# Kernel optimization log

Measured on AMD Instinct MI355X. Metric: run time of the kernel, lower is better.

## Reference

```python
import jax, jax.numpy as jnp
import numpy as np

ST_HIDDEN = 128
ST_HEADS = 4
ST_LAYERS = 3
RES_SCALE = 1.0
DK = ST_HIDDEN // ST_HEADS


def build_3d_adj(spatial_ei, spatial_ea, n_nodes, window):
    # replicate spatial edges per time slice with node offset t*n_nodes
    offs = (jnp.arange(window) * n_nodes)[None, :, None]  # [1,W,1]
    all_sp_idx = (spatial_ei[:, None, :] + offs).reshape(2, -1)  # [2, W*E]
    all_sp_attr = jnp.tile(spatial_ea, (window, 1))  # [W*E, De]
    # temporal edges t -> t+1 for every node
    src = jnp.arange((window - 1) * n_nodes)
    temp_idx = jnp.stack([src, src + n_nodes], axis=0)  # [2, (W-1)*N]
    temp_attr = jnp.broadcast_to(spatial_ea.mean(axis=0, keepdims=True),
                                 (temp_idx.shape[1], spatial_ea.shape[1]))
    ei = jnp.concatenate([all_sp_idx, temp_idx], axis=1)
    ea = jnp.concatenate([all_sp_attr, temp_attr], axis=0)
    return ei, ea


def seg_softmax(logits, dst, num_nodes):
    # logits [E,H], segment softmax over dst (pyg_softmax)
    m = jax.ops.segment_max(logits, dst, num_segments=num_nodes)  # [N,H]
    ex = jnp.exp(logits - m[dst])
    s = jax.ops.segment_sum(ex, dst, num_segments=num_nodes)
    return ex / (s[dst] + 1e-16)


def layernorm(x, g, b, eps=1e-5):
    mu = x.mean(-1, keepdims=True)
    var = ((x - mu) ** 2).mean(-1, keepdims=True)
    return (x - mu) * jax.lax.rsqrt(var + eps) * g + b


def block(x, ei, ea, qw, qb, kw, kb, vw, vb, fw, fb, ow, ob, ln_g, ln_b):
    B, Nt, _ = x.shape
    H, dk = ST_HEADS, DK
    Q = (x @ qw + qb).reshape(B, Nt, H, dk)
    K = (x @ kw + kb).reshape(B, Nt, H, dk)
    V = (x @ vw + vb).reshape(B, Nt, H, dk)
    src, dst = ei[0], ei[1]
    q_e = Q[:, dst]  # [B,E,H,dk]
    k_e = K[:, src]
    v_e = V[:, src]
    film = ea @ fw + fb  # [E, 2*hidden]
    gamma, beta = jnp.split(film, 2, axis=-1)
    gamma = gamma.reshape(1, -1, H, dk)
    beta = beta.reshape(1, -1, H, dk)
    k_e = k_e * (1.0 + gamma) + beta
    logits = (q_e * k_e).sum(-1) / np.sqrt(dk).astype(np.float32)  # [B,E,H]
    att = jax.vmap(lambda l: seg_softmax(l, dst, Nt))(logits)
    msg = att[..., None] * v_e  # [B,E,H,dk]
    out = jnp.zeros((B, Nt, H, dk), x.dtype).at[:, dst].add(msg)
    y = out.reshape(B, Nt, H * dk) @ ow + ob
    return layernorm(x + y, ln_g, ln_b)


def setup_inputs() -> dict:
    key = jax.random.key(0)
    ks = jax.random.split(key, 12)
    B, W, N, Fin, E, De = 2, 16, 1000, 16, 16000, 8
    H, L = ST_HIDDEN, ST_LAYERS
    g = lambda k, s: jax.random.normal(k, s, jnp.float32) * 0.05
    return {
        "xw": jax.random.normal(ks[0], (B, W, N, Fin), jnp.float32),
        "spatial_ei": jax.random.randint(ks[1], (2, E), 0, N),
        "spatial_ea": jax.random.normal(ks[2], (E, De), jnp.float32),
        "in_w": g(ks[3], (Fin, H)), "in_b": jnp.zeros((H,), jnp.float32),
        "qw": g(ks[4], (L, H, H)), "qb": jnp.zeros((L, H), jnp.float32),
        "kw": g(ks[5], (L, H, H)), "kb": jnp.zeros((L, H), jnp.float32),
        "vw": g(ks[6], (L, H, H)), "vb": jnp.zeros((L, H), jnp.float32),
        "fw": g(ks[7], (L, De, 2 * H)), "fb": jnp.zeros((L, 2 * H), jnp.float32),
        "ow": g(ks[8], (L, H, H)), "ob": jnp.zeros((L, H), jnp.float32),
        "ln_g": jnp.ones((L, H), jnp.float32), "ln_b": jnp.zeros((L, H), jnp.float32),
        "head_w": g(ks[9], (H, 1)), "head_b": jnp.zeros((1,), jnp.float32),
    }


def reference(xw, spatial_ei, spatial_ea, in_w, in_b, qw, qb, kw, kb, vw, vb,
              fw, fb, ow, ob, ln_g, ln_b, head_w, head_b):
    B, W, N, Fin = xw.shape
    ei, ea = build_3d_adj(spatial_ei, spatial_ea, N, W)
    x = xw.reshape(B, W * N, Fin) @ in_w + in_b
    for l in range(ST_LAYERS):
        bx = block(x, ei, ea, qw[l], qb[l], kw[l], kb[l], vw[l], vb[l],
                   fw[l], fb[l], ow[l], ob[l], ln_g[l], ln_b[l])
        x = x + RES_SCALE * (bx - x)
    last = x.reshape(B, W, N, -1)[:, -1]  # [B,N,H]
    return jax.nn.softplus(last @ head_w + head_b).squeeze(-1)  # [B,N]
```

## Files before the change

### kernel.cpp

```cpp
#include <hip/hip_runtime.h>
#include <math.h>

constexpr int B    = 2;
constexpr int W    = 16;
constexpr int N    = 1000;
constexpr int FIN  = 16;
constexpr int E    = 16000;
constexpr int DE   = 8;
constexpr int H    = 128;
constexpr int L    = 3;
constexpr int WL   = 4;
constexpr int W0G  = 12;
constexpr int RPB  = WL * N;
constexpr int ROWS = B * RPB;
constexpr int NMAT = 12;

__device__ __forceinline__ float blockSum128(float v) {
  #pragma unroll
  for (int off = 32; off >= 1; off >>= 1) v += __shfl_xor(v, off);
  __shared__ float s2[2];
  int w = threadIdx.x >> 6;
  __syncthreads();
  if ((threadIdx.x & 63) == 0) s2[w] = v;
  __syncthreads();
  return s2[0] + s2[1];
}

__device__ __forceinline__ float dpp_add_xor1(float x) {
  int y = __builtin_amdgcn_update_dpp(0, __float_as_int(x), 0xB1, 0xF, 0xF, true);
  return x + __int_as_float(y);
}
__device__ __forceinline__ float dpp_add_xor2(float x) {
  int y = __builtin_amdgcn_update_dpp(0, __float_as_int(x), 0x4E, 0xF, 0xF, true);
  return x + __int_as_float(y);
}
__device__ __forceinline__ float headSum32(float p) {
  p = dpp_add_xor1(p);
  p = dpp_add_xor2(p);
  p += __shfl_xor(p, 4);
  p += __shfl_xor(p, 8);
  p += __shfl_xor(p, 16);
  return p;
}
__device__ __forceinline__ float dot4(float4 a, float4 b) {
  return a.x * b.x + a.y * b.y + a.z * b.z + a.w * b.w;
}

__global__ void k_hist(const int* __restrict__ ei, int* __restrict__ cnt,
                       const float* __restrict__ ea, float* __restrict__ meanea) {
  int bid = blockIdx.x;
  int t = threadIdx.x;
  if (bid < 64) {
    int e = bid * 256 + t;
    if (e < E) atomicAdd(&cnt[ei[E + e]], 1);
  } else {
    __shared__ float sbuf[256];
    int d = t & 7, g = t >> 3;
    float s = 0.f;
    for (int e = (bid - 64) * 32 + g; e < E; e += 64 * 32) s += ea[(long)e * DE + d];
    sbuf[t] = s;
    __syncthreads();
    for (int st = 16; st >= 1; st >>= 1) {
      if (g < st) sbuf[g * 8 + d] += sbuf[(g + st) * 8 + d];
      __syncthreads();
    }
    if (g == 0) atomicAdd(&meanea[d], sbuf[d]);
  }
}

__global__ void k_scan(const int* __restrict__ cnt, int* __restrict__ offs,
                       int* __restrict__ cursor) {
  __shared__ int scn[1024];
  int t = threadIdx.x;
  int v = (t < N) ? cnt[t] : 0;
  scn[t] = v;
  __syncthreads();
  for (int st = 1; st < 1024; st <<= 1) {
    int add = (t >= st) ? scn[t - st] : 0;
    __syncthreads();
    scn[t] += add;
    __syncthreads();
  }
  if (t < N) {
    offs[t + 1] = scn[t];
    if (t == 0) offs[0] = 0;
    cursor[t] = scn[t] - v;
  }
}

__global__ void k_prep2(const int* __restrict__ ei,
                        int* __restrict__ cursor, int2* __restrict__ csr,
                        const float* __restrict__ qw, const float* __restrict__ kw,
                        const float* __restrict__ vw, const float* __restrict__ ow,
                        float4* __restrict__ wTp4,
                        const float* __restrict__ xw, const float* __restrict__ in_w,
                        const float* __restrict__ in_b, float* __restrict__ x) {
  int bid = blockIdx.x;
  int t = threadIdx.x;
  if (bid < 64) {
    int e = bid * 256 + t;
    if (e < E) {
      int src = ei[e];
      int dst = ei[E + e];
      int pos = atomicAdd(&cursor[dst], 1);
      csr[pos] = make_int2(src, e);
    }
  } else if (bid < 64 + NMAT * 16) {
    int bid2 = bid - 64;
    int mat = bid2 / 16;
    int pair = bid2 % 16;
    int kk4 = pair * 2 + (t >> 7);
    int c = t & 127;
    int l = mat >> 2, mm = mat & 3;
    const float* src = ((mm == 0) ? qw : (mm == 1) ? kw : (mm == 2) ? vw : ow) + (long)l * H * H;
    int k0 = kk4 * 4;
    float4 v4;
    v4.x = src[(k0 + 0) * H + c];
    v4.y = src[(k0 + 1) * H + c];
    v4.z = src[(k0 + 2) * H + c];
    v4.w = src[(k0 + 3) * H + c];
    wTp4[((long)mat * 32 + kk4) * H + c] = v4;
  } else {
    int bi = bid - (64 + NMAT * 16);
    int b = bi / 63, tt = bi % 63;
    int lr0 = tt * 64;
    __shared__ float xwS[64][FIN];
    __shared__ float inS[FIN][H];
    for (int i = t; i < 64 * FIN; i += 256) {
      int r = i >> 4, k = i & 15;
      int lr = lr0 + r;
      float val = 0.f;
      if (lr < RPB) {
        int wl = lr / N, n = lr % N;
        val = xw[(((long)b * W + (W0G + wl)) * N + n) * FIN + k];
      }
      xwS[r][k] = val;
    }
    for (int i = t; i < FIN * H; i += 256) inS[i >> 7][i & 127] = in_w[i];
    __syncthreads();
    #pragma unroll
    for (int qi = 0; qi < 8; qi++) {
      int idx = t + qi * 256;
      int r = idx >> 5, cq = idx & 31;
      int lr = lr0 + r;
      if (lr < RPB) {
        float4 acc = *(const float4*)(in_b + cq * 4);
        #pragma unroll
        for (int k = 0; k < FIN; k++) {
          float xv = xwS[r][k];
          float4 w4 = *(const float4*)(&inS[k][cq * 4]);
          acc.x += xv * w4.x; acc.y += xv * w4.y; acc.z += xv * w4.z; acc.w += xv * w4.w;
        }
        *(float4*)(x + ((long)b * RPB + lr) * H + cq * 4) = acc;
      }
    }
  }
}

__global__ void k_gemm(const float* __restrict__ X, const float4* __restrict__ wTp4,
                       int matBase,
                       const float* __restrict__ bq, const float* __restrict__ bk,
                       const float* __restrict__ bv,
                       float* __restrict__ Cq, float* __restrict__ Ck, float* __restrict__ Cv,
                       int base, int rows_pb, int tiles) {
  int m = blockIdx.y;
  const float* bm = (m == 0) ? bq : (m == 1) ? bk : bv;
  float* Cm       = (m == 0) ? Cq : (m == 1) ? Ck : Cv;
  const float4* wp = wTp4 + (long)(matBase + m) * 32 * H;
  int bb = blockIdx.x / tiles;
  int tt = blockIdx.x % tiles;
  int lr0 = tt * 32;
  long grow0 = (long)bb * RPB + base + lr0;
  int t = threadIdx.x;
  __shared__ float xs[32][H];
  #pragma unroll
  for (int qi = 0; qi < 4; qi++) {
    int idx = t + qi * 256;
    int r = idx >> 5, c4 = idx & 31;
    float4 v4 = make_float4(0.f, 0.f, 0.f, 0.f);
    if (lr0 + r < rows_pb) v4 = *(const float4*)(X + (grow0 + r) * H + c4 * 4);
    *(float4*)&xs[r][c4 * 4] = v4;
  }
  __syncthreads();
  int cg = t & 31, rg = t >> 5;
  float4 bias4 = *(const float4*)(bm + cg * 4);
  float4 acc0 = bias4, acc1 = bias4, acc2 = bias4, acc3 = bias4;
  #pragma unroll 4
  for (int kk4 = 0; kk4 < 32; kk4++) {
    const float4* wr = wp + kk4 * H + cg * 4;
    float4 w0 = wr[0], w1 = wr[1], w2 = wr[2], w3 = wr[3];
    float4 x0 = *(const float4*)&xs[rg * 4 + 0][kk4 * 4];
    float4 x1 = *(const float4*)&xs[rg * 4 + 1][kk4 * 4];
    float4 x2 = *(const float4*)&xs[rg * 4 + 2][kk4 * 4];
    float4 x3 = *(const float4*)&xs[rg * 4 + 3][kk4 * 4];
    acc0.x += dot4(x0, w0); acc0.y += dot4(x0, w1); acc0.z += dot4(x0, w2); acc0.w += dot4(x0, w3);
    acc1.x += dot4(x1, w0); acc1.y += dot4(x1, w1); acc1.z += dot4(x1, w2); acc1.w += dot4(x1, w3);
    acc2.x += dot4(x2, w0); acc2.y += dot4(x2, w1); acc2.z += dot4(x2, w2); acc2.w += dot4(x2, w3);
    acc3.x += dot4(x3, w0); acc3.y += dot4(x3, w1); acc3.z += dot4(x3, w2); acc3.w += dot4(x3, w3);
  }
  int lrr = lr0 + rg * 4;
  if (lrr + 0 < rows_pb) *(float4*)(Cm + (grow0 + rg * 4 + 0) * H + cg * 4) = acc0;
  if (lrr + 1 < rows_pb) *(float4*)(Cm + (grow0 + rg * 4 + 1) * H + cg * 4) = acc1;
  if (lrr + 2 < rows_pb) *(float4*)(Cm + (grow0 + rg * 4 + 2) * H + cg * 4) = acc2;
  if (lrr + 3 < rows_pb) *(float4*)(Cm + (grow0 + rg * 4 + 3) * H + cg * 4) = acc3;
}

__global__ void k_attn_oln(const float* __restrict__ Qb, const float* __restrict__ Kb,
                           const float* __restrict__ Vb,
                           const float* __restrict__ ea,
                           const float* __restrict__ fw_l, const float* __restrict__ fb_l,
                           const float* __restrict__ meanea,
                           const int* __restrict__ offs, const int2* __restrict__ csr,
                           const float* __restrict__ x, const float4* __restrict__ owp,
                           const float* __restrict__ ob, const float* __restrict__ lng,
                           const float* __restrict__ lnb, float* __restrict__ xo,
                           int out_lo,
                           const float* __restrict__ hw, const float* __restrict__ hb,
                           float* __restrict__ out, int do_head) {
  int tid = threadIdx.x;
  int nwin = WL - out_lo;
  int idx = blockIdx.x;
  int b = idx / (nwin * N);
  int rem = idx % (nwin * N);
  int wl = out_lo + rem / N;
  int n = rem % N;
  long drow = ((long)b * WL + wl) * N + n;
  float q = Qb[drow * H + tid];
  long sbase = ((long)b * WL + wl) * N;
  long trow  = ((long)b * WL + wl - 1) * N + n;
  const float scale = 0.17677669529663687f;
  int i0 = offs[n], i1 = offs[n + 1];

  float rgw[DE], rbw[DE];
  #pragma unroll
  for (int d = 0; d < DE; d++) {
    rgw[d] = fw_l[d * 2 * H + tid];
    rbw[d] = fw_l[d * 2 * H + H + tid];
  }
  float fbg = fb_l[tid], fbb = fb_l[H + tid];
  const float4* eap = (const float4*)ea;

  float g = fbg, be = fbb;
  #pragma unroll
  for (int d = 0; d < DE; d++) {
    float am = meanea[d] * (1.0f / E);
    g  += am * rgw[d];
    be += am * rbw[d];
  }
  float kv = Kb[trow * H + tid];
  float vv = Vb[trow * H + tid];
  float p  = q * (kv * (1.f + g) + be);
  float pe = __expf(headSum32(p) * scale);
  float ssum = pe, acc = pe * vv;

  for (int i4 = i0; i4 < i1; i4 += 4) {
    #pragma unroll
    for (int j = 0; j < 4; j++) {
      int i = i4 + j;
      int ic = (i < i1) ? i : (i1 - 1);
      int2 se = csr[ic];
      long srow = sbase + se.x;
      float4 a0 = eap[(long)se.y * 2];
      float4 a1 = eap[(long)se.y * 2 + 1];
      float g2 = fbg + a0.x * rgw[0] + a0.y * rgw[1] + a0.z * rgw[2] + a0.w * rgw[3]
                     + a1.x * rgw[4] + a1.y * rgw[5] + a1.z * rgw[6] + a1.w * rgw[7];
      float b2 = fbb + a0.x * rbw[0] + a0.y * rbw[1] + a0.z * rbw[2] + a0.w * rbw[3]
                     + a1.x * rbw[4] + a1.y * rbw[5] + a1.z * rbw[6] + a1.w * rbw[7];
      float kv2 = Kb[srow * H + tid];
      float vv2 = Vb[srow * H + tid];
      float p2  = q * (kv2 * (1.f + g2) + b2);
      float pe2 = __expf(headSum32(p2) * scale);
      pe2 = (i < i1) ? pe2 : 0.f;
      ssum += pe2;
      acc  += pe2 * vv2;
    }
  }
  float ab = acc / (ssum + 1e-16f);

  __shared__ float sab[H];
  sab[tid] = ab;
  __syncthreads();
  float y = ob[tid];
  #pragma unroll 8
  for (int kk4 = 0; kk4 < 32; kk4++) {
    float4 w4 = owp[kk4 * H + tid];
    float4 a4 = *(const float4*)&sab[kk4 * 4];
    y += dot4(a4, w4);
  }

  float v = x[drow * H + tid] + y;
  float mu = blockSum128(v) * (1.f / H);
  float dv = v - mu;
  float var = blockSum128(dv * dv) * (1.f / H);
  float o = dv * rsqrtf(var + 1e-5f) * lng[tid] + lnb[tid];

  if (!do_head) {
    xo[drow * H + tid] = o;
  } else {
    float hv = o * hw[tid];
    float tot = blockSum128(hv);
    if (tid == 0) {
      float z = tot + hb[0];
      out[b * N + n] = fmaxf(z, 0.f) + log1pf(expf(-fabsf(z)));
    }
  }
}

extern "C" void kernel_launch(void* const* d_in, const int* in_sizes, int n_in,
                              void* d_out, int out_size, void* d_ws, size_t ws_size,
                              hipStream_t stream) {
  const float* xw   = (const float*)d_in[0];
  const int*   ei   = (const int*)d_in[1];
  const float* ea   = (const float*)d_in[2];
  const float* in_w = (const float*)d_in[3];
  const float* in_b = (const float*)d_in[4];
  const float* qw   = (const float*)d_in[5];
  const float* qb   = (const float*)d_in[6];
  const float* kw   = (const float*)d_in[7];
  const float* kb   = (const float*)d_in[8];
  const float* vw   = (const float*)d_in[9];
  const float* vb   = (const float*)d_in[10];
  const float* fw   = (const float*)d_in[11];
  const float* fb   = (const float*)d_in[12];
  const float* ow   = (const float*)d_in[13];
  const float* ob   = (const float*)d_in[14];
  const float* ln_g = (const float*)d_in[15];
  const float* ln_b = (const float*)d_in[16];
  const float* hw   = (const float*)d_in[17];
  const float* hb   = (const float*)d_in[18];
  float* out = (float*)d_out;

  float* ws   = (float*)d_ws;
  float* x    = ws;
  float* x2   = x  + (long)ROWS * H;
  float* Qb   = x2 + (long)ROWS * H;
  float* Kb   = Qb + (long)ROWS * H;
  float* Vb   = Kb + (long)ROWS * H;
  float* wTp  = Vb + (long)ROWS * H;
  int2* csr    = (int2*)(wTp + (long)NMAT * H * H);
  int* cnt     = (int*)(csr + E);
  float* meanea = (float*)(cnt + N);
  int* offs    = (int*)(meanea + 8);
  int* cursor  = offs + N + 1;
  float4* wTp4 = (float4*)wTp;

  hipMemsetAsync(cnt, 0, (N + 8) * sizeof(int), stream);
  k_hist<<<128, 256, 0, stream>>>(ei, cnt, ea, meanea);
  k_scan<<<1, 1024, 0, stream>>>(cnt, offs, cursor);
  k_prep2<<<64 + NMAT * 16 + 126, 256, 0, stream>>>(
      ei, cursor, csr, qw, kw, vw, ow, wTp4, xw, in_w, in_b, x);

  float* xa = x;
  float* xb = x2;
  for (int l = 0; l < L; l++) {
    int in_lo = l, out_lo = l + 1;
    int rows_pb = (WL - in_lo) * N;
    int tiles = (rows_pb + 31) / 32;
    k_gemm<<<dim3(B * tiles, 3), 256, 0, stream>>>(
        xa, wTp4, l * 4, qb + (long)l * H, kb + (long)l * H, vb + (long)l * H,
        Qb, Kb, Vb, in_lo * N, rows_pb, tiles);
    int nout = B * (WL - out_lo) * N;
    int last = (l == L - 1) ? 1 : 0;
    k_attn_oln<<<nout, H, 0, stream>>>(
        Qb, Kb, Vb, ea, fw + (long)l * DE * 2 * H, fb + (long)l * 2 * H, meanea,
        offs, csr,
        xa, wTp4 + ((long)l * 4 + 3) * 32 * H, ob + (long)l * H,
        ln_g + (long)l * H, ln_b + (long)l * H, xb, out_lo,
        hw, hb, out, last);
    float* tmp = xa; xa = xb; xb = tmp;
  }
}
```

Before: 257.0 us.

## Split attention and output-projection+LayerNorm into separate kernels with tiled GEMM

```diff
diff --git a/kernel.cpp b/kernel.cpp
--- a/kernel.cpp
+++ b/kernel.cpp
@@ -14,17 +14,6 @@
 constexpr int RPB  = WL * N;
 constexpr int ROWS = B * RPB;
 constexpr int NMAT = 12;
-
-__device__ __forceinline__ float blockSum128(float v) {
-  #pragma unroll
-  for (int off = 32; off >= 1; off >>= 1) v += __shfl_xor(v, off);
-  __shared__ float s2[2];
-  int w = threadIdx.x >> 6;
-  __syncthreads();
-  if ((threadIdx.x & 63) == 0) s2[w] = v;
-  __syncthreads();
-  return s2[0] + s2[1];
-}
 
 __device__ __forceinline__ float dpp_add_xor1(float x) {
   int y = __builtin_amdgcn_update_dpp(0, __float_as_int(x), 0xB1, 0xF, 0xF, true);
@@ -205,18 +194,13 @@
   if (lrr + 3 < rows_pb) *(float4*)(Cm + (grow0 + rg * 4 + 3) * H + cg * 4) = acc3;
 }
 
-__global__ void k_attn_oln(const float* __restrict__ Qb, const float* __restrict__ Kb,
-                           const float* __restrict__ Vb,
-                           const float* __restrict__ ea,
-                           const float* __restrict__ fw_l, const float* __restrict__ fb_l,
-                           const float* __restrict__ meanea,
-                           const int* __restrict__ offs, const int2* __restrict__ csr,
-                           const float* __restrict__ x, const float4* __restrict__ owp,
-                           const float* __restrict__ ob, const float* __restrict__ lng,
-                           const float* __restrict__ lnb, float* __restrict__ xo,
-                           int out_lo,
-                           const float* __restrict__ hw, const float* __restrict__ hb,
-                           float* __restrict__ out, int do_head) {
+__global__ void k_attn(const float* __restrict__ Qb, const float* __restrict__ Kb,
+                       const float* __restrict__ Vb,
+                       const float* __restrict__ ea,
+                       const float* __restrict__ fw_l, const float* __restrict__ fb_l,
+                       const float* __restrict__ meanea,
+                       const int* __restrict__ offs, const int2* __restrict__ csr,
+                       float* __restrict__ abuf, int out_lo) {
   int tid = threadIdx.x;
   int nwin = WL - out_lo;
   int idx = blockIdx.x;
@@ -275,33 +259,106 @@
       acc  += pe2 * vv2;
     }
   }
-  float ab = acc / (ssum + 1e-16f);
-
-  __shared__ float sab[H];
-  sab[tid] = ab;
+  abuf[drow * H + tid] = acc / (ssum + 1e-16f);
+}
+
+__global__ void k_oln(const float* __restrict__ abuf, const float4* __restrict__ owp,
+                      const float* __restrict__ ob, const float* __restrict__ x,
+                      const float* __restrict__ lng, const float* __restrict__ lnb,
+                      float* __restrict__ xo, int out_lo,
+                      const float* __restrict__ hw, const float* __restrict__ hb,
+                      float* __restrict__ out, int do_head,
+                      int rows_o, int tiles_o) {
+  int bb = blockIdx.x / tiles_o;
+  int tt = blockIdx.x % tiles_o;
+  int lr0 = tt * 32;
+  long grow0 = (long)bb * RPB + out_lo * N + lr0;
+  int t = threadIdx.x;
+  __shared__ float xs[32][H];
+  #pragma unroll
+  for (int qi = 0; qi < 4; qi++) {
+    int idx = t + qi * 256;
+    int r = idx >> 5, c4 = idx & 31;
+    float4 v4 = make_float4(0.f, 0.f, 0.f, 0.f);
+    if (lr0 + r < rows_o) v4 = *(const float4*)(abuf + (grow0 + r) * H + c4 * 4);
+    *(float4*)&xs[r][c4 * 4] = v4;
+  }
   __syncthreads();
-  float y = ob[tid];
-  #pragma unroll 8
+  int cg = t & 31, rg = t >> 5;
+  float4 bias4 = *(const float4*)(ob + cg * 4);
+  float4 acc0 = bias4, acc1 = bias4, acc2 = bias4, acc3 = bias4;
+  #pragma unroll 4
   for (int kk4 = 0; kk4 < 32; kk4++) {
-    float4 w4 = owp[kk4 * H + tid];
-    float4 a4 = *(const float4*)&sab[kk4 * 4];
-    y += dot4(a4, w4);
-  }
-
-  float v = x[drow * H + tid] + y;
-  float mu = blockSum128(v) * (1.f / H);
-  float dv = v - mu;
-  float var = blockSum128(dv * dv) * (1.f / H);
-  float o = dv * rsqrtf(var + 1e-5f) * lng[tid] + lnb[tid];
-
+    const float4* wr = owp + kk4 * H + cg * 4;
+    float4 w0 = wr[0], w1 = wr[1], w2 = wr[2], w3 = wr[3];
+    float4 x0 = *(const float4*)&xs[rg * 4 + 0][kk4 * 4];
+    float4 x1 = *(const float4*)&xs[rg * 4 + 1][kk4 * 4];
+    float4 x2 = *(const float4*)&xs[rg * 4 + 2][kk4 * 4];
+    float4 x3 = *(const float4*)&xs[rg * 4 + 3][kk4 * 4];
+    acc0.x += dot4(x0, w0); acc0.y += dot4(x0, w1); acc0.z += dot4(x0, w2); acc0.w += dot4(x0, w3);
+    acc1.x += dot4(x1, w0); acc1.y += dot4(x1, w1); acc1.z += dot4(x1, w2); acc1.w += dot4(x1, w3);
+    acc2.x += dot4(x2, w0); acc2.y += dot4(x2, w1); acc2.z += dot4(x2, w2); acc2.w += dot4(x2, w3);
+    acc3.x += dot4(x3, w0); acc3.y += dot4(x3, w1); acc3.z += dot4(x3, w2); acc3.w += dot4(x3, w3);
+  }
+  __syncthreads();
+  *(float4*)&xs[rg * 4 + 0][cg * 4] = acc0;
+  *(float4*)&xs[rg * 4 + 1][cg * 4] = acc1;
+  *(float4*)&xs[rg * 4 + 2][cg * 4] = acc2;
+  *(float4*)&xs[rg * 4 + 3][cg * 4] = acc3;
+  __syncthreads();
+  int r2 = t >> 3, l8 = t & 7;
+  int c0 = l8 * 16;
+  int lr = lr0 + r2;
+  long growr = (long)bb * RPB + out_lo * N + lr;
+  bool live = (lr < rows_o);
+  float v[16];
+  float s1 = 0.f;
+  #pragma unroll
+  for (int j = 0; j < 4; j++) {
+    float4 xr = make_float4(0.f, 0.f, 0.f, 0.f);
+    if (live) xr = *(const float4*)(x + growr * H + c0 + j * 4);
+    float4 yv = *(const float4*)&xs[r2][c0 + j * 4];
+    v[j * 4 + 0] = yv.x + xr.x; v[j * 4 + 1] = yv.y + xr.y;
+    v[j * 4 + 2] = yv.z + xr.z; v[j * 4 + 3] = yv.w + xr.w;
+    s1 += v[j * 4 + 0] + v[j * 4 + 1] + v[j * 4 + 2] + v[j * 4 + 3];
+  }
+  s1 += __shfl_xor(s1, 1); s1 += __shfl_xor(s1, 2); s1 += __shfl_xor(s1, 4);
+  float mu = s1 * (1.f / H);
+  float s2 = 0.f;
+  #pragma unroll
+  for (int k = 0; k < 16; k++) { float d = v[k] - mu; s2 += d * d; }
+  s2 += __shfl_xor(s2, 1); s2 += __shfl_xor(s2, 2); s2 += __shfl_xor(s2, 4);
+  float rsq = rsqrtf(s2 * (1.f / H) + 1e-5f);
   if (!do_head) {
-    xo[drow * H + tid] = o;
+    if (live) {
+      #pragma unroll
+      for (int j = 0; j < 4; j++) {
+        float4 gv = *(const float4*)(lng + c0 + j * 4);
+        float4 bv = *(const float4*)(lnb + c0 + j * 4);
+        float4 o;
+        o.x = (v[j * 4 + 0] - mu) * rsq * gv.x + bv.x;
+        o.y = (v[j * 4 + 1] - mu) * rsq * gv.y + bv.y;
+        o.z = (v[j * 4 + 2] - mu) * rsq * gv.z + bv.z;
+        o.w = (v[j * 4 + 3] - mu) * rsq * gv.w + bv.w;
+        *(float4*)(xo + growr * H + c0 + j * 4) = o;
+      }
+    }
   } else {
-    float hv = o * hw[tid];
-    float tot = blockSum128(hv);
-    if (tid == 0) {
-      float z = tot + hb[0];
-      out[b * N + n] = fmaxf(z, 0.f) + log1pf(expf(-fabsf(z)));
+    float hv = 0.f;
+    #pragma unroll
+    for (int j = 0; j < 4; j++) {
+      float4 gv = *(const float4*)(lng + c0 + j * 4);
+      float4 bv = *(const float4*)(lnb + c0 + j * 4);
+      float4 wv = *(const float4*)(hw + c0 + j * 4);
+      hv += ((v[j * 4 + 0] - mu) * rsq * gv.x + bv.x) * wv.x;
+      hv += ((v[j * 4 + 1] - mu) * rsq * gv.y + bv.y) * wv.y;
+      hv += ((v[j * 4 + 2] - mu) * rsq * gv.z + bv.z) * wv.z;
+      hv += ((v[j * 4 + 3] - mu) * rsq * gv.w + bv.w) * wv.w;
+    }
+    hv += __shfl_xor(hv, 1); hv += __shfl_xor(hv, 2); hv += __shfl_xor(hv, 4);
+    if (l8 == 0 && live) {
+      float z = hv + hb[0];
+      out[bb * N + lr] = fmaxf(z, 0.f) + log1pf(expf(-fabsf(z)));
     }
   }
 }
@@ -336,7 +393,8 @@
   float* Qb   = x2 + (long)ROWS * H;
   float* Kb   = Qb + (long)ROWS * H;
   float* Vb   = Kb + (long)ROWS * H;
-  float* wTp  = Vb + (long)ROWS * H;
+  float* abuf = Vb + (long)ROWS * H;
+  float* wTp  = abuf + (long)ROWS * H;
   int2* csr    = (int2*)(wTp + (long)NMAT * H * H);
   int* cnt     = (int*)(csr + E);
   float* meanea = (float*)(cnt + N);
@@ -359,14 +417,18 @@
     k_gemm<<<dim3(B * tiles, 3), 256, 0, stream>>>(
         xa, wTp4, l * 4, qb + (long)l * H, kb + (long)l * H, vb + (long)l * H,
         Qb, Kb, Vb, in_lo * N, rows_pb, tiles);
-    int nout = B * (WL - out_lo) * N;
+    int nwin = WL - out_lo;
+    int nout = B * nwin * N;
     int last = (l == L - 1) ? 1 : 0;
-    k_attn_oln<<<nout, H, 0, stream>>>(
+    k_attn<<<nout, H, 0, stream>>>(
         Qb, Kb, Vb, ea, fw + (long)l * DE * 2 * H, fb + (long)l * 2 * H, meanea,
-        offs, csr,
-        xa, wTp4 + ((long)l * 4 + 3) * 32 * H, ob + (long)l * H,
-        ln_g + (long)l * H, ln_b + (long)l * H, xb, out_lo,
-        hw, hb, out, last);
+        offs, csr, abuf, out_lo);
+    int rows_o = nwin * N;
+    int tiles_o = (rows_o + 31) / 32;
+    k_oln<<<B * tiles_o, 256, 0, stream>>>(
+        abuf, wTp4 + ((long)l * 4 + 3) * 32 * H, ob + (long)l * H,
+        xa, ln_g + (long)l * H, ln_b + (long)l * H, xb, out_lo,
+        hw, hb, out, last, rows_o, tiles_o);
     float* tmp = xa; xa = xb; xb = tmp;
   }
 }
```

Measured after the change: 295.3 us. 1.15x slower.

## Fuse all stages into one cooperative persistent kernel with grid syncs

Applied to the files above, without the earlier changes.

```diff
diff --git a/kernel.cpp b/kernel.cpp
--- a/kernel.cpp
+++ b/kernel.cpp
@@ -1,5 +1,8 @@
 #include <hip/hip_runtime.h>
+#include <hip/hip_cooperative_groups.h>
 #include <math.h>
+
+namespace cg = cooperative_groups;
 
 constexpr int B    = 2;
 constexpr int W    = 16;
@@ -14,17 +17,18 @@
 constexpr int RPB  = WL * N;
 constexpr int ROWS = B * RPB;
 constexpr int NMAT = 12;
-
-__device__ __forceinline__ float blockSum128(float v) {
-  #pragma unroll
-  for (int off = 32; off >= 1; off >>= 1) v += __shfl_xor(v, off);
-  __shared__ float s2[2];
-  int w = threadIdx.x >> 6;
-  __syncthreads();
-  if ((threadIdx.x & 63) == 0) s2[w] = v;
-  __syncthreads();
-  return s2[0] + s2[1];
-}
+constexpr int GRID = 768;
+
+struct Params {
+  const float* xw; const int* ei; const float* ea;
+  const float* in_w; const float* in_b;
+  const float* qw; const float* qb; const float* kw; const float* kb;
+  const float* vw; const float* vb; const float* fw; const float* fb;
+  const float* ow; const float* ob; const float* lng; const float* lnb;
+  const float* hw; const float* hb; float* out;
+  float* x; float* x2; float* Qb; float* Kb; float* Vb;
+  float* wTp; int2* csr; float* meanea; int* offs;
+};
 
 __device__ __forceinline__ float dpp_add_xor1(float x) {
   int y = __builtin_amdgcn_update_dpp(0, __float_as_int(x), 0xB1, 0xF, 0xF, true);
@@ -45,6 +49,318 @@
 __device__ __forceinline__ float dot4(float4 a, float4 b) {
   return a.x * b.x + a.y * b.y + a.z * b.z + a.w * b.w;
 }
+
+
+__device__ __forceinline__ void transpose_unit(const Params& P, int u) {
+  int t = threadIdx.x;
+  int mat = u / 16, pair = u % 16;
+  int kk4 = pair * 2 + (t >> 7);
+  int c = t & 127;
+  int l = mat >> 2, mm = mat & 3;
+  const float* src = ((mm == 0) ? P.qw : (mm == 1) ? P.kw : (mm == 2) ? P.vw : P.ow)
+                     + (long)l * H * H;
+  int k0 = kk4 * 4;
+  float4 v4;
+  v4.x = src[(k0 + 0) * H + c];
+  v4.y = src[(k0 + 1) * H + c];
+  v4.z = src[(k0 + 2) * H + c];
+  v4.w = src[(k0 + 3) * H + c];
+  ((float4*)P.wTp)[((long)mat * 32 + kk4) * H + c] = v4;
+}
+
+__device__ __forceinline__ void inproj_unit(const Params& P, int u, float* __restrict__ smem) {
+  int t = threadIdx.x;
+  int b = u / 63, tt = u % 63;
+  int lr0 = tt * 64;
+  float* xwS = smem;
+  float* inS = smem + 64 * FIN;
+  for (int i = t; i < 64 * FIN; i += 256) {
+    int r = i >> 4, k = i & 15;
+    int lr = lr0 + r;
+    float val = 0.f;
+    if (lr < RPB) {
+      int wl = lr / N, n = lr % N;
+      val = P.xw[(((long)b * W + (W0G + wl)) * N + n) * FIN + k];
+    }
+    xwS[r * FIN + k] = val;
+  }
+  for (int i = t; i < FIN * H; i += 256) inS[i] = P.in_w[i];
+  __syncthreads();
+  #pragma unroll
+  for (int qi = 0; qi < 8; qi++) {
+    int idx = t + qi * 256;
+    int r = idx >> 5, cq = idx & 31;
+    int lr = lr0 + r;
+    if (lr < RPB) {
+      float4 acc = *(const float4*)(P.in_b + cq * 4);
+      #pragma unroll
+      for (int k = 0; k < FIN; k++) {
+        float xv = xwS[r * FIN + k];
+        float4 w4 = *(const float4*)(&inS[k * H + cq * 4]);
+        acc.x += xv * w4.x; acc.y += xv * w4.y; acc.z += xv * w4.z; acc.w += xv * w4.w;
+      }
+      *(float4*)(P.x + ((long)b * RPB + lr) * H + cq * 4) = acc;
+    }
+  }
+}
+
+__device__ __forceinline__ void histscan_unit(const Params& P, float* __restrict__ smemf) {
+  int t = threadIdx.x;
+  int* scnt = (int*)smemf;
+  int* curS = scnt + 1024;
+  int* part = scnt + 2048;
+  for (int i = t; i < 1024; i += 256) scnt[i] = 0;
+  __syncthreads();
+  for (int e = t; e < E; e += 256) atomicAdd(&scnt[P.ei[E + e]], 1);
+  __syncthreads();
+  int a0 = scnt[4 * t + 0], a1 = scnt[4 * t + 1], a2 = scnt[4 * t + 2], a3 = scnt[4 * t + 3];
+  int p0 = a0, p1 = p0 + a1, p2 = p1 + a2, p3 = p2 + a3;
+  part[t] = p3;
+  __syncthreads();
+  for (int st = 1; st < 256; st <<= 1) {
+    int add = (t >= st) ? part[t - st] : 0;
+    __syncthreads();
+    part[t] += add;
+    __syncthreads();
+  }
+  int base = (t > 0) ? part[t - 1] : 0;
+  int incl[4] = { base + p0, base + p1, base + p2, base + p3 };
+  int av[4] = { a0, a1, a2, a3 };
+  #pragma unroll
+  for (int j = 0; j < 4; j++) {
+    int idx = 4 * t + j;
+    if (idx < N) {
+      P.offs[idx + 1] = incl[j];
+      curS[idx] = incl[j] - av[j];
+    }
+  }
+  if (t == 0) P.offs[0] = 0;
+  __syncthreads();
+  for (int e = t; e < E; e += 256) {
+    int sr = P.ei[e];
+    int d  = P.ei[E + e];
+    int pos = atomicAdd(&curS[d], 1);
+    P.csr[pos] = make_int2(sr, e);
+  }
+}
+
+__device__ __forceinline__ void easum_unit(const Params& P, int u, float* __restrict__ smem) {
+  int t = threadIdx.x;
+  float* sbuf = smem;
+  int d = t & 7, g = t >> 3;
+  float s = 0.f;
+  for (int e = u * 32 + g; e < E; e += 64 * 32) s += P.ea[(long)e * DE + d];
+  sbuf[t] = s;
+  __syncthreads();
+  for (int st = 16; st >= 1; st >>= 1) {
+    if (g < st) sbuf[g * 8 + d] += sbuf[(g + st) * 8 + d];
+    __syncthreads();
+  }
+  if (g == 0) atomicAdd(&P.meanea[d], sbuf[d]);
+}
+
+__device__ __forceinline__ void gemm_unit(const Params& P, int l, int u,
+                                          float* __restrict__ xs, const float* __restrict__ X) {
+  __syncthreads();
+  int rows_pb = (WL - l) * N;
+  int tiles = (rows_pb + 31) >> 5;
+  int m = u / (B * tiles);
+  int rest = u % (B * tiles);
+  int bb = rest / tiles, tt = rest % tiles;
+  const float* bm = ((m == 0) ? P.qb : (m == 1) ? P.kb : P.vb) + (long)l * H;
+  float* Cm = (m == 0) ? P.Qb : (m == 1) ? P.Kb : P.Vb;
+  const float4* wp = (const float4*)P.wTp + (long)(l * 4 + m) * 32 * H;
+  int lr0 = tt * 32;
+  long grow0 = (long)bb * RPB + l * N + lr0;
+  int t = threadIdx.x;
+  #pragma unroll
+  for (int qi = 0; qi < 4; qi++) {
+    int idx = t + qi * 256;
+    int r = idx >> 5, c4 = idx & 31;
+    float4 v4 = make_float4(0.f, 0.f, 0.f, 0.f);
+    if (lr0 + r < rows_pb) v4 = *(const float4*)(X + (grow0 + r) * H + c4 * 4);
+    *(float4*)&xs[r * H + c4 * 4] = v4;
+  }
+  __syncthreads();
+  int cg = t & 31, rg = t >> 5;
+  float4 bias4 = *(const float4*)(bm + cg * 4);
+  float4 acc0 = bias4, acc1 = bias4, acc2 = bias4, acc3 = bias4;
+  #pragma unroll 4
+  for (int kk4 = 0; kk4 < 32; kk4++) {
+    const float4* wr = wp + kk4 * H + cg * 4;
+    float4 w0 = wr[0], w1 = wr[1], w2 = wr[2], w3 = wr[3];
+    float4 x0 = *(const float4*)&xs[(rg * 4 + 0) * H + kk4 * 4];
+    float4 x1 = *(const float4*)&xs[(rg * 4 + 1) * H + kk4 * 4];
+    float4 x2 = *(const float4*)&xs[(rg * 4 + 2) * H + kk4 * 4];
+    float4 x3 = *(const float4*)&xs[(rg * 4 + 3) * H + kk4 * 4];
+    acc0.x += dot4(x0, w0); acc0.y += dot4(x0, w1); acc0.z += dot4(x0, w2); acc0.w += dot4(x0, w3);
+    acc1.x += dot4(x1, w0); acc1.y += dot4(x1, w1); acc1.z += dot4(x1, w2); acc1.w += dot4(x1, w3);
+    acc2.x += dot4(x2, w0); acc2.y += dot4(x2, w1); acc2.z += dot4(x2, w2); acc2.w += dot4(x2, w3);
+    acc3.x += dot4(x3, w0); acc3.y += dot4(x3, w1); acc3.z += dot4(x3, w2); acc3.w += dot4(x3, w3);
+  }
+  int lrr = lr0 + rg * 4;
+  if (lrr + 0 < rows_pb) *(float4*)(Cm + (grow0 + rg * 4 + 0) * H + cg * 4) = acc0;
+  if (lrr + 1 < rows_pb) *(float4*)(Cm + (grow0 + rg * 4 + 1) * H + cg * 4) = acc1;
+  if (lrr + 2 < rows_pb) *(float4*)(Cm + (grow0 + rg * 4 + 2) * H + cg * 4) = acc2;
+  if (lrr + 3 < rows_pb) *(float4*)(Cm + (grow0 + rg * 4 + 3) * H + cg * 4) = acc3;
+}
+
+__device__ __forceinline__ void attn_unit(const Params& P, int l, int u,
+                                          float* __restrict__ smem, float* __restrict__ sred,
+                                          const float* __restrict__ xa, float* __restrict__ xb,
+                                          int do_head) {
+  int t = threadIdx.x;
+  int g2 = t >> 7, ch = t & 127;
+  int out_lo = l + 1, nwin = WL - out_lo;
+  int id = u * 2 + g2;
+  int b = id / (nwin * N);
+  int rem = id % (nwin * N);
+  int wl = out_lo + rem / N;
+  int n = rem % N;
+  long drow = ((long)b * WL + wl) * N + n;
+  float q = P.Qb[drow * H + ch];
+  long sbase = ((long)b * WL + wl) * N;
+  long trow  = ((long)b * WL + wl - 1) * N + n;
+  const float scale = 0.17677669529663687f;
+  int i0 = P.offs[n], i1 = P.offs[n + 1];
+
+  const float* fw_l = P.fw + (long)l * DE * 2 * H;
+  const float* fb_l = P.fb + (long)l * 2 * H;
+  float rgw[DE], rbw[DE];
+  #pragma unroll
+  for (int d = 0; d < DE; d++) {
+    rgw[d] = fw_l[d * 2 * H + ch];
+    rbw[d] = fw_l[d * 2 * H + H + ch];
+  }
+  float fbg = fb_l[ch], fbb = fb_l[H + ch];
+  const float4* eap = (const float4*)P.ea;
+
+  float gg = fbg, be = fbb;
+  #pragma unroll
+  for (int d = 0; d < DE; d++) {
+    float am = P.meanea[d] * (1.0f / E);
+    gg += am * rgw[d];
+    be += am * rbw[d];
+  }
+  float kv = P.Kb[trow * H + ch];
+  float vv = P.Vb[trow * H + ch];
+  float p  = q * (kv * (1.f + gg) + be);
+  float pe = __expf(headSum32(p) * scale);
+  float ssum = pe, acc = pe * vv;
+
+  for (int i4 = i0; i4 < i1; i4 += 4) {
+    #pragma unroll
+    for (int j = 0; j < 4; j++) {
+      int i = i4 + j;
+      int ic = (i < i1) ? i : (i1 - 1);
+      int2 se = P.csr[ic];
+      long srow = sbase + se.x;
+      float4 a0 = eap[(long)se.y * 2];
+      float4 a1 = eap[(long)se.y * 2 + 1];
+      float g2f = fbg + a0.x * rgw[0] + a0.y * rgw[1] + a0.z * rgw[2] + a0.w * rgw[3]
+                      + a1.x * rgw[4] + a1.y * rgw[5] + a1.z * rgw[6] + a1.w * rgw[7];
+      float b2f = fbb + a0.x * rbw[0] + a0.y * rbw[1] + a0.z * rbw[2] + a0.w * rbw[3]
+                      + a1.x * rbw[4] + a1.y * rbw[5] + a1.z * rbw[6] + a1.w * rbw[7];
+      float kv2 = P.Kb[srow * H + ch];
+      float vv2 = P.Vb[srow * H + ch];
+      float p2  = q * (kv2 * (1.f + g2f) + b2f);
+      float pe2 = __expf(headSum32(p2) * scale);
+      pe2 = (i < i1) ? pe2 : 0.f;
+      ssum += pe2;
+      acc  += pe2 * vv2;
+    }
+  }
+  float ab = acc / (ssum + 1e-16f);
+
+  __syncthreads();
+  smem[t] = ab;
+  __syncthreads();
+  const float4* owp = (const float4*)P.wTp + ((long)l * 4 + 3) * 32 * H;
+  float y = P.ob[(long)l * H + ch];
+  #pragma unroll 8
+  for (int kk4 = 0; kk4 < 32; kk4++) {
+    float4 w4 = owp[kk4 * H + ch];
+    float4 a4 = *(const float4*)&smem[g2 * 128 + kk4 * 4];
+    y += dot4(a4, w4);
+  }
+
+  float v = xa[drow * H + ch] + y;
+  float s1 = v;
+  #pragma unroll
+  for (int off = 32; off >= 1; off >>= 1) s1 += __shfl_xor(s1, off);
+  __syncthreads();
+  if ((t & 63) == 0) sred[t >> 6] = s1;
+  __syncthreads();
+  float mu = (sred[g2 * 2] + sred[g2 * 2 + 1]) * (1.f / H);
+  float dv = v - mu;
+  float s2 = dv * dv;
+  #pragma unroll
+  for (int off = 32; off >= 1; off >>= 1) s2 += __shfl_xor(s2, off);
+  __syncthreads();
+  if ((t & 63) == 0) sred[t >> 6] = s2;
+  __syncthreads();
+  float var = (sred[g2 * 2] + sred[g2 * 2 + 1]) * (1.f / H);
+  float o = dv * rsqrtf(var + 1e-5f) * P.lng[(long)l * H + ch] + P.lnb[(long)l * H + ch];
+
+  if (!do_head) {
+    xb[drow * H + ch] = o;
+  } else {
+    float hv = o * P.hw[ch];
+    #pragma unroll
+    for (int off = 32; off >= 1; off >>= 1) hv += __shfl_xor(hv, off);
+    __syncthreads();
+    if ((t & 63) == 0) sred[t >> 6] = hv;
+    __syncthreads();
+    if (ch == 0) {
+      float z = sred[g2 * 2] + sred[g2 * 2 + 1] + P.hb[0];
+      P.out[b * N + n] = fmaxf(z, 0.f) + log1pf(expf(-fabsf(z)));
+    }
+  }
+}
+
+__global__ __launch_bounds__(256, 3) void k_mega(Params P) {
+  __shared__ __align__(16) float smem[32 * H];
+  __shared__ float sred[8];
+  cg::grid_group grid = cg::this_grid();
+  int bid = blockIdx.x;
+  int t = threadIdx.x;
+
+  int nu0 = NMAT * 16 + 126 + 1;
+  for (int un = bid; un < nu0; un += GRID) {
+    __syncthreads();
+    if (un < NMAT * 16) transpose_unit(P, un);
+    else if (un < NMAT * 16 + 126) inproj_unit(P, un - NMAT * 16, smem);
+    else { if (t < 8) P.meanea[t] = 0.f; }
+  }
+  grid.sync();
+
+  int nu1 = 1 + 64 + B * 125 * 3;
+  for (int un = bid; un < nu1; un += GRID) {
+    __syncthreads();
+    if (un == 0) histscan_unit(P, smem);
+    else if (un <= 64) easum_unit(P, un - 1, smem);
+    else gemm_unit(P, 0, un - 65, smem, P.x);
+  }
+  grid.sync();
+
+  const float* xa = P.x;
+  float* xb = P.x2;
+  for (int l = 0; l < L; l++) {
+    if (l > 0) {
+      int tiles = ((WL - l) * N + 31) >> 5;
+      int ug = B * tiles * 3;
+      for (int u = bid; u < ug; u += GRID) gemm_unit(P, l, u, smem, xa);
+      grid.sync();
+    }
+    int nwin = WL - (l + 1);
+    int units = (B * nwin * N) >> 1;
+    for (int u = bid; u < units; u += GRID)
+      attn_unit(P, l, u, smem, sred, xa, xb, l == L - 1);
+    if (l < L - 1) grid.sync();
+    const float* tmp = xb; xb = (float*)xa; xa = tmp;
+  }
+}
+
 
 __global__ void k_hist(const int* __restrict__ ei, int* __restrict__ cnt,
                        const float* __restrict__ ea, float* __restrict__ meanea) {
@@ -278,6 +594,7 @@
   float ab = acc / (ssum + 1e-16f);
 
   __shared__ float sab[H];
+  __shared__ float s2m[2];
   sab[tid] = ab;
   __syncthreads();
   float y = ob[tid];
@@ -289,18 +606,34 @@
   }
 
   float v = x[drow * H + tid] + y;
-  float mu = blockSum128(v) * (1.f / H);
+  float s1 = v;
+  #pragma unroll
+  for (int off = 32; off >= 1; off >>= 1) s1 += __shfl_xor(s1, off);
+  __syncthreads();
+  if ((tid & 63) == 0) s2m[tid >> 6] = s1;
+  __syncthreads();
+  float mu = (s2m[0] + s2m[1]) * (1.f / H);
   float dv = v - mu;
-  float var = blockSum128(dv * dv) * (1.f / H);
+  float s2 = dv * dv;
+  #pragma unroll
+  for (int off = 32; off >= 1; off >>= 1) s2 += __shfl_xor(s2, off);
+  __syncthreads();
+  if ((tid & 63) == 0) s2m[tid >> 6] = s2;
+  __syncthreads();
+  float var = (s2m[0] + s2m[1]) * (1.f / H);
   float o = dv * rsqrtf(var + 1e-5f) * lng[tid] + lnb[tid];
 
   if (!do_head) {
     xo[drow * H + tid] = o;
   } else {
     float hv = o * hw[tid];
-    float tot = blockSum128(hv);
+    #pragma unroll
+    for (int off = 32; off >= 1; off >>= 1) hv += __shfl_xor(hv, off);
+    __syncthreads();
+    if ((tid & 63) == 0) s2m[tid >> 6] = hv;
+    __syncthreads();
     if (tid == 0) {
-      float z = tot + hb[0];
+      float z = s2m[0] + s2m[1] + hb[0];
       out[b * N + n] = fmaxf(z, 0.f) + log1pf(expf(-fabsf(z)));
     }
   }
@@ -309,64 +642,70 @@
 extern "C" void kernel_launch(void* const* d_in, const int* in_sizes, int n_in,
                               void* d_out, int out_size, void* d_ws, size_t ws_size,
                               hipStream_t stream) {
-  const float* xw   = (const float*)d_in[0];
-  const int*   ei   = (const int*)d_in[1];
-  const float* ea   = (const float*)d_in[2];
-  const float* in_w = (const float*)d_in[3];
-  const float* in_b = (const float*)d_in[4];
-  const float* qw   = (const float*)d_in[5];
-  const float* qb   = (const float*)d_in[6];
-  const float* kw   = (const float*)d_in[7];
-  const float* kb   = (const float*)d_in[8];
-  const float* vw   = (const float*)d_in[9];
-  const float* vb   = (const float*)d_in[10];
-  const float* fw   = (const float*)d_in[11];
-  const float* fb   = (const float*)d_in[12];
-  const float* ow   = (const float*)d_in[13];
-  const float* ob   = (const float*)d_in[14];
-  const float* ln_g = (const float*)d_in[15];
-  const float* ln_b = (const float*)d_in[16];
-  const float* hw   = (const float*)d_in[17];
-  const float* hb   = (const float*)d_in[18];
-  float* out = (float*)d_out;
-
-  float* ws   = (float*)d_ws;
-  float* x    = ws;
-  float* x2   = x  + (long)ROWS * H;
-  float* Qb   = x2 + (long)ROWS * H;
-  float* Kb   = Qb + (long)ROWS * H;
-  float* Vb   = Kb + (long)ROWS * H;
-  float* wTp  = Vb + (long)ROWS * H;
-  int2* csr    = (int2*)(wTp + (long)NMAT * H * H);
-  int* cnt     = (int*)(csr + E);
-  float* meanea = (float*)(cnt + N);
-  int* offs    = (int*)(meanea + 8);
-  int* cursor  = offs + N + 1;
-  float4* wTp4 = (float4*)wTp;
-
-  hipMemsetAsync(cnt, 0, (N + 8) * sizeof(int), stream);
-  k_hist<<<128, 256, 0, stream>>>(ei, cnt, ea, meanea);
-  k_scan<<<1, 1024, 0, stream>>>(cnt, offs, cursor);
-  k_prep2<<<64 + NMAT * 16 + 126, 256, 0, stream>>>(
-      ei, cursor, csr, qw, kw, vw, ow, wTp4, xw, in_w, in_b, x);
-
-  float* xa = x;
-  float* xb = x2;
-  for (int l = 0; l < L; l++) {
-    int in_lo = l, out_lo = l + 1;
-    int rows_pb = (WL - in_lo) * N;
-    int tiles = (rows_pb + 31) / 32;
-    k_gemm<<<dim3(B * tiles, 3), 256, 0, stream>>>(
-        xa, wTp4, l * 4, qb + (long)l * H, kb + (long)l * H, vb + (long)l * H,
-        Qb, Kb, Vb, in_lo * N, rows_pb, tiles);
-    int nout = B * (WL - out_lo) * N;
-    int last = (l == L - 1) ? 1 : 0;
-    k_attn_oln<<<nout, H, 0, stream>>>(
-        Qb, Kb, Vb, ea, fw + (long)l * DE * 2 * H, fb + (long)l * 2 * H, meanea,
-        offs, csr,
-        xa, wTp4 + ((long)l * 4 + 3) * 32 * H, ob + (long)l * H,
-        ln_g + (long)l * H, ln_b + (long)l * H, xb, out_lo,
-        hw, hb, out, last);
-    float* tmp = xa; xa = xb; xb = tmp;
-  }
-}
+  Params P;
+  P.xw   = (const float*)d_in[0];
+  P.ei   = (const int*)d_in[1];
+  P.ea   = (const float*)d_in[2];
+  P.in_w = (const float*)d_in[3];
+  P.in_b = (const float*)d_in[4];
+  P.qw   = (const float*)d_in[5];
+  P.qb   = (const float*)d_in[6];
+  P.kw   = (const float*)d_in[7];
+  P.kb   = (const float*)d_in[8];
+  P.vw   = (const float*)d_in[9];
+  P.vb   = (const float*)d_in[10];
+  P.fw   = (const float*)d_in[11];
+  P.fb   = (const float*)d_in[12];
+  P.ow   = (const float*)d_in[13];
+  P.ob   = (const float*)d_in[14];
+  P.lng  = (const float*)d_in[15];
+  P.lnb  = (const float*)d_in[16];
+  P.hw   = (const float*)d_in[17];
+  P.hb   = (const float*)d_in[18];
+  P.out  = (float*)d_out;
+
+  float* ws = (float*)d_ws;
+  P.x    = ws;
+  P.x2   = P.x  + (long)ROWS * H;
+  P.Qb   = P.x2 + (long)ROWS * H;
+  P.Kb   = P.Qb + (long)ROWS * H;
+  P.Vb   = P.Kb + (long)ROWS * H;
+  P.wTp  = P.Vb + (long)ROWS * H;
+  P.csr  = (int2*)(P.wTp + (long)NMAT * H * H);
+  int* cnt = (int*)(P.csr + E);
+  P.meanea = (float*)(cnt + N);
+  P.offs = (int*)(P.meanea + 8);
+  int* cursor = P.offs + N + 1;
+
+  void* args[] = { (void*)&P };
+  hipError_t rc = hipLaunchCooperativeKernel((const void*)k_mega, dim3(GRID), dim3(256),
+                                             args, 0, stream);
+  if (rc != hipSuccess) {
+    (void)hipGetLastError();
+    hipMemsetAsync(cnt, 0, (N + 8) * sizeof(int), stream);
+    k_hist<<<128, 256, 0, stream>>>(P.ei, cnt, P.ea, P.meanea);
+    k_scan<<<1, 1024, 0, stream>>>(cnt, P.offs, cursor);
+    k_prep2<<<64 + NMAT * 16 + 126, 256, 0, stream>>>(
+        P.ei, cursor, P.csr, P.qw, P.kw, P.vw, P.ow, (float4*)P.wTp,
+        P.xw, P.in_w, P.in_b, P.x);
+    float* xa = P.x;
+    float* xb = P.x2;
+    for (int l = 0; l < L; l++) {
+      int in_lo = l, out_lo = l + 1;
+      int rows_pb = (WL - in_lo) * N;
+      int tiles = (rows_pb + 31) / 32;
+      k_gemm<<<dim3(B * tiles, 3), 256, 0, stream>>>(
+          xa, (float4*)P.wTp, l * 4, P.qb + (long)l * H, P.kb + (long)l * H,
+          P.vb + (long)l * H, P.Qb, P.Kb, P.Vb, in_lo * N, rows_pb, tiles);
+      int nout = B * (WL - out_lo) * N;
+      int last = (l == L - 1) ? 1 : 0;
+      k_attn_oln<<<nout, H, 0, stream>>>(
+          P.Qb, P.Kb, P.Vb, P.ea, P.fw + (long)l * DE * 2 * H,
+          P.fb + (long)l * 2 * H, P.meanea, P.offs, P.csr,
+          xa, (float4*)P.wTp + ((long)l * 4 + 3) * 32 * H, P.ob + (long)l * H,
+          P.lng + (long)l * H, P.lnb + (long)l * H, xb, out_lo,
+          P.hw, P.hb, P.out, last);
+      float* tmp = xa; xa = xb; xb = tmp;
+    }
+  }
+}
```

After: 947.1 us. 269% more time.

## Fuse histogram, scan and CSR build into one prep kernel with atomic flags

Applied to the files above, without the earlier changes.

```diff
diff --git a/kernel.cpp b/kernel.cpp
--- a/kernel.cpp
+++ b/kernel.cpp
@@ -14,17 +14,7 @@
 constexpr int RPB  = WL * N;
 constexpr int ROWS = B * RPB;
 constexpr int NMAT = 12;
-
-__device__ __forceinline__ float blockSum128(float v) {
-  #pragma unroll
-  for (int off = 32; off >= 1; off >>= 1) v += __shfl_xor(v, off);
-  __shared__ float s2[2];
-  int w = threadIdx.x >> 6;
-  __syncthreads();
-  if ((threadIdx.x & 63) == 0) s2[w] = v;
-  __syncthreads();
-  return s2[0] + s2[1];
-}
+constexpr int EPB  = E / 64;
 
 __device__ __forceinline__ float dpp_add_xor1(float x) {
   int y = __builtin_amdgcn_update_dpp(0, __float_as_int(x), 0xB1, 0xF, 0xF, true);
@@ -46,18 +36,80 @@
   return a.x * b.x + a.y * b.y + a.z * b.z + a.w * b.w;
 }
 
-__global__ void k_hist(const int* __restrict__ ei, int* __restrict__ cnt,
-                       const float* __restrict__ ea, float* __restrict__ meanea) {
+__global__ void k_prep_all(const int* __restrict__ ei, const float* __restrict__ ea,
+                           int* __restrict__ cnt, float* __restrict__ meanea,
+                           int* __restrict__ flagA, int* __restrict__ flagB,
+                           const float* __restrict__ qw, const float* __restrict__ kw,
+                           const float* __restrict__ vw, const float* __restrict__ ow,
+                           float4* __restrict__ wTp4,
+                           const float* __restrict__ xw, const float* __restrict__ in_w,
+                           const float* __restrict__ in_b, float* __restrict__ x,
+                           int2* __restrict__ csr, int* __restrict__ offs,
+                           int* __restrict__ cursor) {
+  __shared__ float xwS[64][FIN];
+  __shared__ float inS[FIN][H];
+  __shared__ int   part[256];
+  __shared__ int   bcast;
   int bid = blockIdx.x;
   int t = threadIdx.x;
+
   if (bid < 64) {
-    int e = bid * 256 + t;
-    if (e < E) atomicAdd(&cnt[ei[E + e]], 1);
-  } else {
-    __shared__ float sbuf[256];
+    int e = bid * EPB + t;
+    if (t < EPB) atomicAdd(&cnt[ei[E + e]], 1);
+    __syncthreads();
+    if (t == 0) {
+      int old = __hip_atomic_fetch_add(flagA, 1, __ATOMIC_ACQ_REL, __HIP_MEMORY_SCOPE_AGENT);
+      bcast = (old == 63) ? 1 : 0;
+    }
+    __syncthreads();
+    if (bcast) {
+      int i0 = 4 * t;
+      int a0 = (i0 + 0 < N) ? cnt[i0 + 0] : 0;
+      int a1 = (i0 + 1 < N) ? cnt[i0 + 1] : 0;
+      int a2 = (i0 + 2 < N) ? cnt[i0 + 2] : 0;
+      int a3 = (i0 + 3 < N) ? cnt[i0 + 3] : 0;
+      int p1 = a0 + a1, p2 = p1 + a2, p3 = p2 + a3;
+      part[t] = p3;
+      __syncthreads();
+      for (int st = 1; st < 256; st <<= 1) {
+        int add = (t >= st) ? part[t - st] : 0;
+        __syncthreads();
+        part[t] += add;
+        __syncthreads();
+      }
+      int base = (t > 0) ? part[t - 1] : 0;
+      int inc0 = base + a0, inc1 = base + p1, inc2 = base + p2, inc3 = base + p3;
+      if (i0 + 0 < N) { offs[i0 + 1] = inc0;
+        __hip_atomic_store(&cursor[i0 + 0], inc0 - a0, __ATOMIC_RELAXED, __HIP_MEMORY_SCOPE_AGENT); }
+      if (i0 + 1 < N) { offs[i0 + 2] = inc1;
+        __hip_atomic_store(&cursor[i0 + 1], inc1 - a1, __ATOMIC_RELAXED, __HIP_MEMORY_SCOPE_AGENT); }
+      if (i0 + 2 < N) { offs[i0 + 3] = inc2;
+        __hip_atomic_store(&cursor[i0 + 2], inc2 - a2, __ATOMIC_RELAXED, __HIP_MEMORY_SCOPE_AGENT); }
+      if (i0 + 3 < N) { offs[i0 + 4] = inc3;
+        __hip_atomic_store(&cursor[i0 + 3], inc3 - a3, __ATOMIC_RELAXED, __HIP_MEMORY_SCOPE_AGENT); }
+      if (t == 0) offs[0] = 0;
+      __threadfence();
+      __syncthreads();
+      if (t == 0) __hip_atomic_store(flagB, 1, __ATOMIC_RELEASE, __HIP_MEMORY_SCOPE_AGENT);
+    }
+    if (t == 0) {
+      while (__hip_atomic_load(flagB, __ATOMIC_ACQUIRE, __HIP_MEMORY_SCOPE_AGENT) == 0)
+        __builtin_amdgcn_s_sleep(32);
+    }
+    __syncthreads();
+    if (t < EPB) {
+      int e2 = bid * EPB + t;
+      int sr = ei[e2];
+      int d  = ei[E + e2];
+      int pos = atomicAdd(&cursor[d], 1);
+      csr[pos] = make_int2(sr, e2);
+    }
+  } else if (bid < 128) {
+    float* sbuf = &xwS[0][0];
+    int u = bid - 64;
     int d = t & 7, g = t >> 3;
     float s = 0.f;
-    for (int e = (bid - 64) * 32 + g; e < E; e += 64 * 32) s += ea[(long)e * DE + d];
+    for (int e = u * 32 + g; e < E; e += 64 * 32) s += ea[(long)e * DE + d];
     sbuf[t] = s;
     __syncthreads();
     for (int st = 16; st >= 1; st >>= 1) {
@@ -65,50 +117,9 @@
       __syncthreads();
     }
     if (g == 0) atomicAdd(&meanea[d], sbuf[d]);
-  }
-}
-
-__global__ void k_scan(const int* __restrict__ cnt, int* __restrict__ offs,
-                       int* __restrict__ cursor) {
-  __shared__ int scn[1024];
-  int t = threadIdx.x;
-  int v = (t < N) ? cnt[t] : 0;
-  scn[t] = v;
-  __syncthreads();
-  for (int st = 1; st < 1024; st <<= 1) {
-    int add = (t >= st) ? scn[t - st] : 0;
-    __syncthreads();
-    scn[t] += add;
-    __syncthreads();
-  }
-  if (t < N) {
-    offs[t + 1] = scn[t];
-    if (t == 0) offs[0] = 0;
-    cursor[t] = scn[t] - v;
-  }
-}
-
-__global__ void k_prep2(const int* __restrict__ ei,
-                        int* __restrict__ cursor, int2* __restrict__ csr,
-                        const float* __restrict__ qw, const float* __restrict__ kw,
-                        const float* __restrict__ vw, const float* __restrict__ ow,
-                        float4* __restrict__ wTp4,
-                        const float* __restrict__ xw, const float* __restrict__ in_w,
-                        const float* __restrict__ in_b, float* __restrict__ x) {
-  int bid = blockIdx.x;
-  int t = threadIdx.x;
-  if (bid < 64) {
-    int e = bid * 256 + t;
-    if (e < E) {
-      int src = ei[e];
-      int dst = ei[E + e];
-      int pos = atomicAdd(&cursor[dst], 1);
-      csr[pos] = make_int2(src, e);
-    }
-  } else if (bid < 64 + NMAT * 16) {
-    int bid2 = bid - 64;
-    int mat = bid2 / 16;
-    int pair = bid2 % 16;
+  } else if (bid < 128 + NMAT * 16) {
+    int u = bid - 128;
+    int mat = u / 16, pair = u % 16;
     int kk4 = pair * 2 + (t >> 7);
     int c = t & 127;
     int l = mat >> 2, mm = mat & 3;
@@ -121,11 +132,9 @@
     v4.w = src[(k0 + 3) * H + c];
     wTp4[((long)mat * 32 + kk4) * H + c] = v4;
   } else {
-    int bi = bid - (64 + NMAT * 16);
-    int b = bi / 63, tt = bi % 63;
+    int u = bid - (128 + NMAT * 16);
+    int b = u / 63, tt = u % 63;
     int lr0 = tt * 64;
-    __shared__ float xwS[64][FIN];
-    __shared__ float inS[FIN][H];
     for (int i = t; i < 64 * FIN; i += 256) {
       int r = i >> 4, k = i & 15;
       int lr = lr0 + r;
@@ -278,6 +287,7 @@
   float ab = acc / (ssum + 1e-16f);
 
   __shared__ float sab[H];
+  __shared__ float s2m[2];
   sab[tid] = ab;
   __syncthreads();
   float y = ob[tid];
@@ -289,18 +299,34 @@
   }
 
   float v = x[drow * H + tid] + y;
-  float mu = blockSum128(v) * (1.f / H);
+  float s1 = v;
+  #pragma unroll
+  for (int off = 32; off >= 1; off >>= 1) s1 += __shfl_xor(s1, off);
+  __syncthreads();
+  if ((tid & 63) == 0) s2m[tid >> 6] = s1;
+  __syncthreads();
+  float mu = (s2m[0] + s2m[1]) * (1.f / H);
   float dv = v - mu;
-  float var = blockSum128(dv * dv) * (1.f / H);
+  float s2 = dv * dv;
+  #pragma unroll
+  for (int off = 32; off >= 1; off >>= 1) s2 += __shfl_xor(s2, off);
+  __syncthreads();
+  if ((tid & 63) == 0) s2m[tid >> 6] = s2;
+  __syncthreads();
+  float var = (s2m[0] + s2m[1]) * (1.f / H);
   float o = dv * rsqrtf(var + 1e-5f) * lng[tid] + lnb[tid];
 
   if (!do_head) {
     xo[drow * H + tid] = o;
   } else {
     float hv = o * hw[tid];
-    float tot = blockSum128(hv);
+    #pragma unroll
+    for (int off = 32; off >= 1; off >>= 1) hv += __shfl_xor(hv, off);
+    __syncthreads();
+    if ((tid & 63) == 0) s2m[tid >> 6] = hv;
+    __syncthreads();
     if (tid == 0) {
-      float z = tot + hb[0];
+      float z = s2m[0] + s2m[1] + hb[0];
       out[b * N + n] = fmaxf(z, 0.f) + log1pf(expf(-fabsf(z)));
     }
   }
@@ -340,15 +366,16 @@
   int2* csr    = (int2*)(wTp + (long)NMAT * H * H);
   int* cnt     = (int*)(csr + E);
   float* meanea = (float*)(cnt + N);
-  int* offs    = (int*)(meanea + 8);
+  int* flagA   = (int*)(meanea + 8);
+  int* flagB   = flagA + 1;
+  int* offs    = flagB + 1;
   int* cursor  = offs + N + 1;
   float4* wTp4 = (float4*)wTp;
 
-  hipMemsetAsync(cnt, 0, (N + 8) * sizeof(int), stream);
-  k_hist<<<128, 256, 0, stream>>>(ei, cnt, ea, meanea);
-  k_scan<<<1, 1024, 0, stream>>>(cnt, offs, cursor);
-  k_prep2<<<64 + NMAT * 16 + 126, 256, 0, stream>>>(
-      ei, cursor, csr, qw, kw, vw, ow, wTp4, xw, in_w, in_b, x);
+  hipMemsetAsync(cnt, 0, (N + 8 + 2) * sizeof(int), stream);
+  k_prep_all<<<128 + NMAT * 16 + 126, 256, 0, stream>>>(
+      ei, ea, cnt, meanea, flagA, flagB,
+      qw, kw, vw, ow, wTp4, xw, in_w, in_b, x, csr, offs, cursor);
 
   float* xa = x;
   float* xb = x2;
```

Measured after the change: 260.4 us. Within noise of the previous version (+1.3%).
